# Performance work log

Hardware: AMD Instinct MI355X
Metric: run time of the kernel (lower is better)

The kernel has to match this reference:

```python
import jax, jax.numpy as jnp
import numpy as np

VOCAB = 50000
EMB = 200        # embedding_size
CAP = 3          # capitalization_size
IN = EMB + CAP   # LSTM input size = 203
HID = 128        # LSTMCell(128)
B = 256
T = 500          # comment_length
NC = 6           # num_classes
DENSE = 64


def _lstm_scan(x_tbi, W, b):
    """x_tbi: [T,B,IN]. W: [IN+HID, 4*HID] (tf gate order i, j, f, o), b: [4*HID].
    Returns h sequence [T,B,HID]. forget_bias=1.0 as in tf.contrib.rnn.LSTMCell."""
    h0 = jnp.zeros((x_tbi.shape[1], HID), x_tbi.dtype)

    def step(carry, x):
        h, c = carry
        gates = jnp.concatenate([x, h], axis=-1) @ W + b   # [B, 4*HID]
        i, j, f, o = jnp.split(gates, 4, axis=-1)
        c = jax.nn.sigmoid(f + 1.0) * c + jax.nn.sigmoid(i) * jnp.tanh(j)
        h = jax.nn.sigmoid(o) * jnp.tanh(c)
        return (h, c), h

    _, hs = jax.lax.scan(step, (h0, h0), x_tbi)
    return hs


def setup_inputs() -> dict:
    key = jax.random.key(0)
    ks = jax.random.split(key, 12)
    words = jax.random.randint(ks[0], (B, T), 0, VOCAB, dtype=jnp.int32)
    capitals = jax.random.randint(ks[1], (B, T), 0, CAP, dtype=jnp.int32)
    # word embeddings: random trainable table with a trailing zero-padding row
    word_emb = jax.random.normal(ks[2], (VOCAB + 1, EMB), dtype=jnp.float32) * 0.1
    # capitalization embedding: one_hot_embedding_matrix(3) = [eye(3); zeros(1,3)]
    cap_emb = jnp.concatenate([jnp.eye(CAP, dtype=jnp.float32),
                               jnp.zeros((1, CAP), dtype=jnp.float32)], axis=0)
    def glorot(k, shape):
        lim = np.sqrt(6.0 / (shape[0] + shape[1]))
        return jax.random.uniform(k, shape, jnp.float32, -lim, lim)
    W_fw = glorot(ks[3], (IN + HID, 4 * HID))
    b_fw = jnp.zeros((4 * HID,), jnp.float32)
    W_bw = glorot(ks[4], (IN + HID, 4 * HID))
    b_bw = jnp.zeros((4 * HID,), jnp.float32)
    W1 = glorot(ks[5], (2 * HID, DENSE))
    b1 = jnp.zeros((DENSE,), jnp.float32)
    W2 = glorot(ks[6], (DENSE, NC))
    b2 = jnp.zeros((NC,), jnp.float32)
    return {"words": words, "capitals": capitals, "word_emb": word_emb,
            "cap_emb": cap_emb, "W_fw": W_fw, "b_fw": b_fw,
            "W_bw": W_bw, "b_bw": b_bw, "W1": W1, "b1": b1,
            "W2": W2, "b2": b2}


def reference(words, capitals, word_emb, cap_emb, W_fw, b_fw, W_bw, b_bw,
              W1, b1, W2, b2):
    # embedding lookups and concat -> [B, T, 203]
    x = jnp.concatenate([word_emb[words], cap_emb[capitals]], axis=-1)
    x_tbi = jnp.transpose(x, (1, 0, 2))                    # [T, B, IN]
    # forward direction: take output at last timestep
    h_fw_last = _lstm_scan(x_tbi, W_fw, b_fw)[-1]          # [B, HID]
    # backward direction: bidirectional_dynamic_rnn reverses bw outputs back,
    # so outputs[1][:, 0, :] == last state of scan over the reversed sequence
    h_bw_first = _lstm_scan(x_tbi[::-1], W_bw, b_bw)[-1]   # [B, HID]
    rnn_output = jnp.concatenate([h_fw_last, h_bw_first], axis=1)  # [B, 256]
    dense1 = jax.nn.elu(rnn_output @ W1 + b1)              # [B, 64]
    y_hat = jax.nn.sigmoid(dense1 @ W2 + b2)               # [B, NC]
    return y_hat
```

## Files before the change

kernel.cpp:

```cpp
#include <hip/hip_runtime.h>

#define T 500
#define NB 256
#define VROWS 50001
#define EMB 200
#define KPAD 224
#define LOG2E 1.44269504f

typedef unsigned short u16;
typedef __attribute__((ext_vector_type(8))) __bf16 bf16x8;
typedef __attribute__((ext_vector_type(8))) short short8;
typedef __attribute__((ext_vector_type(8))) u16 u16x8;
typedef __attribute__((ext_vector_type(4))) float f32x4;
typedef __attribute__((ext_vector_type(4))) u16 u16x4;

__device__ __forceinline__ u16 f2bf(float x) {
  __bf16 h = (__bf16)x;
  return __builtin_bit_cast(u16, h);
}
__device__ __forceinline__ float bf2f(u16 b) {
  union { unsigned u; float f; } v; v.u = ((unsigned)b) << 16;
  return v.f;
}
__device__ __forceinline__ float rcp_(float x) { return __builtin_amdgcn_rcpf(x); }
__device__ __forceinline__ float ex2_(float x) { return __builtin_amdgcn_exp2f(x); }
__device__ __forceinline__ float gsc(int g) { return (g == 1) ? 2.f * LOG2E : -LOG2E; }

__global__ void prep_kernel(const float* __restrict__ cap_emb,
                            const float* __restrict__ Wfw, const float* __restrict__ bfw,
                            const float* __restrict__ Wbw, const float* __restrict__ bbw,
                            float* __restrict__ Cproj, u16* __restrict__ Bt) {
  const int S2 = 2 * 512 * KPAD;
  const int S3 = 2 * 4 * 512;
  int tid = blockIdx.x * blockDim.x + threadIdx.x;
  int nthr = gridDim.x * blockDim.x;
  for (int i = tid; i < S2 + S3; i += nthr) {
    if (i < S2) {
      int d = i / (512 * KPAD), rem = i - d * (512 * KPAD);
      int colp = rem / KPAD, k = rem - colp * KPAD;
      const float* W = d ? Wbw : Wfw;
      int g = colp & 3, jj = colp >> 2;
      Bt[i] = (k < EMB) ? f2bf(W[k * 512 + g * 128 + jj] * gsc(g)) : (u16)0;
    } else {
      int idx = i - S2;
      int dir = idx >> 11; int c = (idx >> 9) & 3; int colp = idx & 511;
      int j = colp >> 2, g = colp & 3;
      const float* W = dir ? Wbw : Wfw;
      const float* bias = dir ? bbw : bfw;
      float v = bias[g * 128 + j] + (g == 2 ? 1.f : 0.f);
      #pragma unroll
      for (int cc = 0; cc < 3; ++cc)
        v += cap_emb[c * 3 + cc] * W[(200 + cc) * 512 + g * 128 + j];
      Cproj[idx] = v * gsc(g);
    }
  }
}

__global__ __launch_bounds__(256) void xproj_kernel(
    const int* __restrict__ words, const int* __restrict__ caps,
    const float* __restrict__ word_emb, const u16* __restrict__ Bt,
    const float* __restrict__ Cproj, u16* __restrict__ XP) {
  const int mt = blockIdx.x, nt = blockIdx.y, dir = blockIdx.z;
  const u16* __restrict__ B = Bt + (size_t)dir * 512 * KPAD;
  const float* __restrict__ Cb = Cproj + dir * 4 * 512;
  u16* __restrict__ xp = XP + (size_t)dir * T * NB * 512;

  __shared__ u16 As[2][128 * 32];
  __shared__ u16 Bs[2][128 * 32];

  const int tid = threadIdx.x;
  const int w = tid >> 6, l = tid & 63;
  const int la = l & 15, lb = l >> 4;
  const int m0 = mt * 128, n0 = nt * 128;
  const int tblk = m0 >> 8;

  const int ar = tid >> 1, ah = tid & 1;
  const int ab = (m0 & 255) + ar;
  const int aword = words[ab * T + tblk];
  const float* __restrict__ aemb = word_emb + (size_t)aword * EMB;

  auto stageA = [&](int buf, int ks) {
    int kbase = ks * 32 + ah * 16;
    u16x8 lo, hi;
    #pragma unroll
    for (int q = 0; q < 4; ++q) {
      int k = kbase + q * 4;
      f32x4 v;
      if (k < EMB) v = *(const f32x4*)(aemb + k);
      else v = f32x4{0.f, 0.f, 0.f, 0.f};
      u16 b0 = f2bf(v[0]), b1 = f2bf(v[1]), b2 = f2bf(v[2]), b3 = f2bf(v[3]);
      if (q < 2) { lo[q*4+0]=b0; lo[q*4+1]=b1; lo[q*4+2]=b2; lo[q*4+3]=b3; }
      else { int qq=q-2; hi[qq*4+0]=b0; hi[qq*4+1]=b1; hi[qq*4+2]=b2; hi[qq*4+3]=b3; }
    }
    *(u16x8*)&As[buf][ar * 32 + ah * 16]     = lo;
    *(u16x8*)&As[buf][ar * 32 + ah * 16 + 8] = hi;
  };
  auto stageB = [&](int buf, int ks) {
    int k0 = ks * 32;
    #pragma unroll
    for (int h = 0; h < 2; ++h) {
      int c = w * 128 + h * 64 + l;
      int row = c >> 2, kq = c & 3;
      const u16* gb = B + (size_t)(n0 + row) * KPAD + k0 + kq * 8;
      __builtin_amdgcn_global_load_lds(
          (const __attribute__((address_space(1))) void*)gb,
          (__attribute__((address_space(3))) void*)&Bs[buf][(w * 128 + h * 64) * 8],
          16, 0, 0);
    }
  };

  f32x4 z = {0.f, 0.f, 0.f, 0.f};
  f32x4 acc[4][4] = {{z,z,z,z},{z,z,z,z},{z,z,z,z},{z,z,z,z}};
  const int wr = w >> 1, wc = w & 1;

  stageA(0, 0); stageB(0, 0);
  __syncthreads();
  #pragma unroll 1
  for (int ks = 0; ks < 7; ++ks) {
    int cur = ks & 1;
    if (ks < 6) { stageA(cur ^ 1, ks + 1); stageB(cur ^ 1, ks + 1); }
    bf16x8 af[4], bfr[4];
    #pragma unroll
    for (int m = 0; m < 4; ++m)
      af[m] = *(const bf16x8*)&As[cur][(wr * 64 + m * 16 + la) * 32 + lb * 8];
    #pragma unroll
    for (int n = 0; n < 4; ++n)
      bfr[n] = *(const bf16x8*)&Bs[cur][(wc * 64 + n * 16 + la) * 32 + lb * 8];
    #pragma unroll
    for (int m = 0; m < 4; ++m)
      #pragma unroll
      for (int n = 0; n < 4; ++n)
        acc[m][n] = __builtin_amdgcn_mfma_f32_16x16x32_bf16(af[m], bfr[n], acc[m][n], 0, 0, 0);
    __syncthreads();
  }

  #pragma unroll
  for (int m = 0; m < 4; ++m) {
    #pragma unroll
    for (int r = 0; r < 4; ++r) {
      int b = (m0 & 255) + wr * 64 + m * 16 + lb * 4 + r;
      int cap = caps[b * T + tblk];
      const float* cbr = Cb + cap * 512;
      u16* op = xp + ((size_t)tblk * NB + b) * 512;
      #pragma unroll
      for (int n = 0; n < 4; ++n) {
        int colp = n0 + wc * 64 + n * 16 + la;
        op[colp] = f2bf(acc[m][n][r] + cbr[colp]);
      }
    }
  }
}

template <int PAR>
__device__ __forceinline__ void lstm_step(
    int t, int dir, int la, int lb, int j,
    const u16* __restrict__ xpd, int voff0, int voff1, int voff2, int voff3,
    const bf16x8 (&bfrag)[4][4], u16* __restrict__ hbuf,
    u16x4 (&xc)[4],
    u16x4 (&xg)[4],
    f32x4& cst, f32x4& hl) {
  const u16* hb = hbuf + PAR * 2048;
  const int swz = (la & 7) << 3;
  bf16x8 afr[4];
  #pragma unroll
  for (int kk = 0; kk < 4; ++kk)
    afr[kk] = *(const bf16x8*)(hb + ((la * 128 + kk * 32 + lb * 8) ^ swz));

  {
    int ts = t + 2; if (ts > T - 1) ts = T - 1;
    int tt = dir ? (T - 1 - ts) : ts;
    const u16* p = xpd + (size_t)tt * (NB * 512);
    xg[0] = *(const u16x4*)(p + voff0);
    xg[1] = *(const u16x4*)(p + voff1);
    xg[2] = *(const u16x4*)(p + voff2);
    xg[3] = *(const u16x4*)(p + voff3);
  }

  f32x4 acc0, acc1, acc2, acc3;
  #pragma unroll
  for (int r = 0; r < 4; ++r) {
    acc0[r] = bf2f(xc[r][0]);
    acc1[r] = bf2f(xc[r][1]);
    acc2[r] = bf2f(xc[r][2]);
    acc3[r] = bf2f(xc[r][3]);
  }
  __builtin_amdgcn_s_setprio(1);
  #pragma unroll
  for (int kk = 0; kk < 4; ++kk) {
    acc0 = __builtin_amdgcn_mfma_f32_16x16x32_bf16(afr[kk], bfrag[0][kk], acc0, 0, 0, 0);
    acc1 = __builtin_amdgcn_mfma_f32_16x16x32_bf16(afr[kk], bfrag[1][kk], acc1, 0, 0, 0);
    acc2 = __builtin_amdgcn_mfma_f32_16x16x32_bf16(afr[kk], bfrag[2][kk], acc2, 0, 0, 0);
    acc3 = __builtin_amdgcn_mfma_f32_16x16x32_bf16(afr[kk], bfrag[3][kk], acc3, 0, 0, 0);
  }
  __builtin_amdgcn_s_setprio(0);
  u16* ho = hbuf + (PAR ^ 1) * 2048;
  #pragma unroll
  for (int r = 0; r < 4; ++r) {
    float ig = rcp_(1.f + ex2_(acc0[r]));
    float tj = 1.f - 2.f * rcp_(1.f + ex2_(acc1[r]));
    float fg = rcp_(1.f + ex2_(acc2[r]));
    float cn = fg * cst[r] + ig * tj;
    cst[r] = cn;
    float og = rcp_(1.f + ex2_(acc3[r]));
    float hn = og * (1.f - 2.f * rcp_(1.f + ex2_(2.f * LOG2E * cn)));
    hl[r] = hn;
    int row = lb * 4 + r;
    ho[(row * 128 + j) ^ ((row & 7) << 3)] = f2bf(hn);
  }
  __builtin_amdgcn_sched_barrier(0);
  asm volatile("s_waitcnt lgkmcnt(0)");
  __builtin_amdgcn_s_barrier();
  __builtin_amdgcn_sched_barrier(0);
}

__global__ __launch_bounds__(512, 1) void lstm_kernel(
    const u16* __restrict__ XP, const float* __restrict__ Wfw,
    const float* __restrict__ Wbw, float* __restrict__ rnn) {
  const int dir = blockIdx.x & 1;
  const int chunk = blockIdx.x >> 1;
  const int b0 = chunk * 16;
  const u16* __restrict__ xpd = XP + (size_t)dir * T * NB * 512;
  const float* __restrict__ W = dir ? Wbw : Wfw;

  const int tid = threadIdx.x;
  const int w = tid >> 6, l = tid & 63, la = l & 15, lb = l >> 4;
  const int j = w * 16 + la;

  const int voff0 = (b0 + lb * 4 + 0) * 512 + j * 4;
  const int voff1 = (b0 + lb * 4 + 1) * 512 + j * 4;
  const int voff2 = (b0 + lb * 4 + 2) * 512 + j * 4;
  const int voff3 = (b0 + lb * 4 + 3) * 512 + j * 4;

  bf16x8 bfrag[4][4];
  #pragma unroll
  for (int g = 0; g < 4; ++g) {
    #pragma unroll
    for (int kk = 0; kk < 4; ++kk) {
      short8 t8;
      #pragma unroll
      for (int r = 0; r < 8; ++r) {
        int k = kk * 32 + lb * 8 + r;
        t8[r] = (short)f2bf(W[(203 + k) * 512 + g * 128 + j] * gsc(g));
      }
      bfrag[g][kk] = __builtin_bit_cast(bf16x8, t8);
    }
  }

  __shared__ u16 hbuf[2 * 16 * 128];
  for (int i = tid; i < 2 * 16 * 128; i += 512) hbuf[i] = 0;

  f32x4 cst = {0.f, 0.f, 0.f, 0.f};
  f32x4 hl  = {0.f, 0.f, 0.f, 0.f};

  u16x4 xA[4], xB[4], xC[4], xD[4];
  {
    int tt0 = dir ? (T - 1) : 0;
    int tt1 = dir ? (T - 2) : 1;
    const u16* p0 = xpd + (size_t)tt0 * (NB * 512);
    const u16* p1 = xpd + (size_t)tt1 * (NB * 512);
    xA[0] = *(const u16x4*)(p0 + voff0); xA[1] = *(const u16x4*)(p0 + voff1);
    xA[2] = *(const u16x4*)(p0 + voff2); xA[3] = *(const u16x4*)(p0 + voff3);
    xB[0] = *(const u16x4*)(p1 + voff0); xB[1] = *(const u16x4*)(p1 + voff1);
    xB[2] = *(const u16x4*)(p1 + voff2); xB[3] = *(const u16x4*)(p1 + voff3);
  }
  __syncthreads();

  #pragma unroll 1
  for (int tq = 0; tq < T / 4; ++tq) {
    int t0 = 4 * tq;
    lstm_step<0>(t0,     dir, la, lb, j, xpd, voff0, voff1, voff2, voff3,
                 bfrag, hbuf, xA, xC, cst, hl);
    lstm_step<1>(t0 + 1, dir, la, lb, j, xpd, voff0, voff1, voff2, voff3,
                 bfrag, hbuf, xB, xD, cst, hl);
    lstm_step<0>(t0 + 2, dir, la, lb, j, xpd, voff0, voff1, voff2, voff3,
                 bfrag, hbuf, xC, xA, cst, hl);
    lstm_step<1>(t0 + 3, dir, la, lb, j, xpd, voff0, voff1, voff2, voff3,
                 bfrag, hbuf, xD, xB, cst, hl);
  }

  #pragma unroll
  for (int r = 0; r < 4; ++r)
    rnn[(size_t)(b0 + lb * 4 + r) * 256 + dir * 128 + j] = hl[r];
}

__global__ void head_kernel(const float* __restrict__ rnn, const float* __restrict__ W1,
                            const float* __restrict__ b1, const float* __restrict__ W2,
                            const float* __restrict__ b2, float* __restrict__ out) {
  int b = blockIdx.x;
  int jj = threadIdx.x;
  __shared__ float d1[64];
  float acc = b1[jj];
  const float* r = rnn + b * 256;
  #pragma unroll 4
  for (int k = 0; k < 256; ++k) acc += r[k] * W1[k * 64 + jj];
  d1[jj] = acc > 0.f ? acc : (__expf(acc) - 1.f);
  __syncthreads();
  if (jj < 6) {
    float a2 = b2[jj];
    #pragma unroll 8
    for (int k = 0; k < 64; ++k) a2 += d1[k] * W2[k * 6 + jj];
    out[b * 6 + jj] = rcp_(1.f + __expf(-a2));
  }
}

extern "C" void kernel_launch(void* const* d_in, const int* in_sizes, int n_in,
                              void* d_out, int out_size, void* d_ws, size_t ws_size,
                              hipStream_t stream) {
  (void)in_sizes; (void)n_in; (void)out_size; (void)ws_size;
  const int*   words    = (const int*)  d_in[0];
  const int*   caps     = (const int*)  d_in[1];
  const float* word_emb = (const float*)d_in[2];
  const float* cap_emb  = (const float*)d_in[3];
  const float* Wfw      = (const float*)d_in[4];
  const float* bfw      = (const float*)d_in[5];
  const float* Wbw      = (const float*)d_in[6];
  const float* bbw      = (const float*)d_in[7];
  const float* W1       = (const float*)d_in[8];
  const float* b1       = (const float*)d_in[9];
  const float* W2       = (const float*)d_in[10];
  const float* b2       = (const float*)d_in[11];
  float* out = (float*)d_out;

  char* base = (char*)d_ws;
  size_t off = 0;
  auto alloc = [&](size_t bytes) {
    char* q = base + off;
    off = (off + bytes + 255) & ~(size_t)255;
    return q;
  };
  u16*   XP     = (u16*)  alloc((size_t)2 * T * NB * 512 * 2);
  u16*   Bt     = (u16*)  alloc((size_t)2 * 512 * KPAD * 2);
  float* Cproj  = (float*)alloc((size_t)2 * 4 * 512 * 4);
  float* rnn    = (float*)alloc((size_t)256 * 256 * 4);

  hipLaunchKernelGGL(prep_kernel, dim3(256), dim3(256), 0, stream,
                     cap_emb, Wfw, bfw, Wbw, bbw, Cproj, Bt);
  hipLaunchKernelGGL(xproj_kernel, dim3(1000, 4, 2), dim3(256), 0, stream,
                     words, caps, word_emb, Bt, Cproj, XP);
  hipLaunchKernelGGL(lstm_kernel, dim3(32), dim3(512), 0, stream,
                     XP, Wfw, Wbw, rnn);
  hipLaunchKernelGGL(head_kernel, dim3(256), dim3(64), 0, stream,
                     rnn, W1, b1, W2, b2, out);
}
```

Before: 700.7 us.

## Pre-convert embeddings to bf16, stage A via async LDS loads, coalesce XP stores

The prep kernel now converts the whole word embedding table to a padded bf16 copy in workspace. The projection GEMM can then gather A rows with global_load_lds instead of per-thread fp32 loads and conversions, and it stages the accumulators through shared memory so each thread writes contiguous 16-byte chunks of XP. The LSTM cell math is also restructured to use fewer reciprocals per step, by combining the sigmoid and tanh denominators. This costs a full-table conversion on every call plus extra shared memory and barriers in the epilogue, and it falls back to the old kernel when the workspace is too small.

```diff
diff --git a/kernel.cpp b/kernel.cpp
--- a/kernel.cpp
+++ b/kernel.cpp
@@ -5,6 +5,7 @@
 #define VROWS 50001
 #define EMB 200
 #define KPAD 224
+#define MPAD 50048
 #define LOG2E 1.44269504f
 
 typedef unsigned short u16;
@@ -14,6 +15,9 @@
 typedef __attribute__((ext_vector_type(4))) float f32x4;
 typedef __attribute__((ext_vector_type(4))) u16 u16x4;
 
+#define AS1 __attribute__((address_space(1)))
+#define AS3 __attribute__((address_space(3)))
+
 __device__ __forceinline__ u16 f2bf(float x) {
   __bf16 h = (__bf16)x;
   return __builtin_bit_cast(u16, h);
@@ -27,9 +31,11 @@
 __device__ __forceinline__ float gsc(int g) { return (g == 1) ? 2.f * LOG2E : -LOG2E; }
 
 __global__ void prep_kernel(const float* __restrict__ cap_emb,
+                            const float* __restrict__ word_emb,
                             const float* __restrict__ Wfw, const float* __restrict__ bfw,
                             const float* __restrict__ Wbw, const float* __restrict__ bbw,
-                            float* __restrict__ Cproj, u16* __restrict__ Bt) {
+                            float* __restrict__ Cproj, u16* __restrict__ Bt,
+                            u16* __restrict__ Apad) {
   const int S2 = 2 * 512 * KPAD;
   const int S3 = 2 * 4 * 512;
   int tid = blockIdx.x * blockDim.x + threadIdx.x;
@@ -54,9 +60,126 @@
       Cproj[idx] = v * gsc(g);
     }
   }
+  if (Apad) {
+    const int S1 = MPAD * (KPAD / 4);
+    for (int i = tid; i < S1; i += nthr) {
+      int v = i / (KPAD / 4), q = i - v * (KPAD / 4);
+      int k = q * 4;
+      u16x4 o;
+      if (v < VROWS && k < EMB) {
+        const float* p = word_emb + (size_t)v * EMB + k;
+        o[0] = f2bf(p[0]); o[1] = f2bf(p[1]); o[2] = f2bf(p[2]); o[3] = f2bf(p[3]);
+      } else {
+        o[0] = o[1] = o[2] = o[3] = 0;
+      }
+      *(u16x4*)(Apad + (size_t)v * KPAD + k) = o;
+    }
+  }
 }
 
 __global__ __launch_bounds__(256) void xproj_kernel(
+    const int* __restrict__ words, const int* __restrict__ caps,
+    const u16* __restrict__ Apad, const u16* __restrict__ Bt,
+    const float* __restrict__ Cproj, u16* __restrict__ XP) {
+  const int mt = blockIdx.x, nt = blockIdx.y, dir = blockIdx.z;
+  const u16* __restrict__ B = Bt + (size_t)dir * 512 * KPAD;
+  u16* __restrict__ xp = XP + (size_t)dir * T * NB * 512;
+
+  __shared__ u16 As[2][128 * 32];
+  __shared__ u16 Bs[2][128 * 32];
+  __shared__ float Cls[64][132];
+
+  const int tid = threadIdx.x;
+  const int w = tid >> 6, l = tid & 63;
+  const int la = l & 15, lb = l >> 4;
+  const int m0 = mt * 128, n0 = nt * 128;
+  const int tblk = m0 >> 8;
+  const int bbase = m0 & 255;
+
+  const int c0 = w * 128 + l, c1 = w * 128 + 64 + l;
+  const int row0 = c0 >> 2, kq0 = c0 & 3;
+  const int row1 = c1 >> 2, kq1 = c1 & 3;
+  const int wd0 = words[(bbase + row0) * T + tblk];
+  const int wd1 = words[(bbase + row1) * T + tblk];
+  const u16* srcA0 = Apad + (size_t)wd0 * KPAD + kq0 * 8;
+  const u16* srcA1 = Apad + (size_t)wd1 * KPAD + kq1 * 8;
+
+  auto stage = [&](int buf, int ks) {
+    __builtin_amdgcn_global_load_lds(
+        (const AS1 void*)(srcA0 + ks * 32),
+        (AS3 void*)&As[buf][(w * 128) * 8], 16, 0, 0);
+    __builtin_amdgcn_global_load_lds(
+        (const AS1 void*)(srcA1 + ks * 32),
+        (AS3 void*)&As[buf][(w * 128 + 64) * 8], 16, 0, 0);
+    int k0 = ks * 32;
+    #pragma unroll
+    for (int h = 0; h < 2; ++h) {
+      int c = w * 128 + h * 64 + l;
+      int row = c >> 2, kq = c & 3;
+      const u16* gb = B + (size_t)(n0 + row) * KPAD + k0 + kq * 8;
+      __builtin_amdgcn_global_load_lds(
+          (const AS1 void*)gb,
+          (AS3 void*)&Bs[buf][(w * 128 + h * 64) * 8], 16, 0, 0);
+    }
+  };
+
+  f32x4 z = {0.f, 0.f, 0.f, 0.f};
+  f32x4 acc[4][4] = {{z,z,z,z},{z,z,z,z},{z,z,z,z},{z,z,z,z}};
+  const int wr = w >> 1, wc = w & 1;
+
+  stage(0, 0);
+  __syncthreads();
+  #pragma unroll 1
+  for (int ks = 0; ks < 7; ++ks) {
+    int cur = ks & 1;
+    if (ks < 6) stage(cur ^ 1, ks + 1);
+    bf16x8 af[4], bfr[4];
+    #pragma unroll
+    for (int m = 0; m < 4; ++m)
+      af[m] = *(const bf16x8*)&As[cur][(wr * 64 + m * 16 + la) * 32 + lb * 8];
+    #pragma unroll
+    for (int n = 0; n < 4; ++n)
+      bfr[n] = *(const bf16x8*)&Bs[cur][(wc * 64 + n * 16 + la) * 32 + lb * 8];
+    #pragma unroll
+    for (int m = 0; m < 4; ++m)
+      #pragma unroll
+      for (int n = 0; n < 4; ++n)
+        acc[m][n] = __builtin_amdgcn_mfma_f32_16x16x32_bf16(af[m], bfr[n], acc[m][n], 0, 0, 0);
+    __syncthreads();
+  }
+
+  const int rrow = tid >> 1, rch = tid & 1;
+  const int rb = bbase + rrow;
+  const int rcap = caps[rb * T + tblk];
+  const float* __restrict__ cbase = Cproj + (dir * 4 + rcap) * 512;
+  u16* __restrict__ rop = xp + ((size_t)tblk * NB + rb) * 512;
+
+  #pragma unroll
+  for (int pass = 0; pass < 2; ++pass) {
+    if (wc == pass) {
+      #pragma unroll
+      for (int m = 0; m < 4; ++m)
+        #pragma unroll
+        for (int n = 0; n < 4; ++n)
+          *(f32x4*)&Cls[n * 16 + la][wr * 64 + m * 16 + lb * 4] = acc[m][n];
+    }
+    __syncthreads();
+    int colp0 = n0 + pass * 64 + rch * 32;
+    #pragma unroll
+    for (int s = 0; s < 4; ++s) {
+      u16x8 o;
+      #pragma unroll
+      for (int e = 0; e < 8; ++e) {
+        int cl = rch * 32 + s * 8 + e;
+        o[e] = f2bf(Cls[cl][rrow] + cbase[colp0 + s * 8 + e]);
+      }
+      *(u16x8*)(rop + colp0 + s * 8) = o;
+    }
+    __syncthreads();
+  }
+}
+
+__global__ __launch_bounds__(256) void xproj_fb_kernel(
     const int* __restrict__ words, const int* __restrict__ caps,
     const float* __restrict__ word_emb, const u16* __restrict__ Bt,
     const float* __restrict__ Cproj, u16* __restrict__ XP) {
@@ -64,21 +187,17 @@
   const u16* __restrict__ B = Bt + (size_t)dir * 512 * KPAD;
   const float* __restrict__ Cb = Cproj + dir * 4 * 512;
   u16* __restrict__ xp = XP + (size_t)dir * T * NB * 512;
-
   __shared__ u16 As[2][128 * 32];
   __shared__ u16 Bs[2][128 * 32];
-
   const int tid = threadIdx.x;
   const int w = tid >> 6, l = tid & 63;
   const int la = l & 15, lb = l >> 4;
   const int m0 = mt * 128, n0 = nt * 128;
   const int tblk = m0 >> 8;
-
   const int ar = tid >> 1, ah = tid & 1;
   const int ab = (m0 & 255) + ar;
   const int aword = words[ab * T + tblk];
   const float* __restrict__ aemb = word_emb + (size_t)aword * EMB;
-
   auto stageA = [&](int buf, int ks) {
     int kbase = ks * 32 + ah * 16;
     u16x8 lo, hi;
@@ -103,16 +222,13 @@
       int row = c >> 2, kq = c & 3;
       const u16* gb = B + (size_t)(n0 + row) * KPAD + k0 + kq * 8;
       __builtin_amdgcn_global_load_lds(
-          (const __attribute__((address_space(1))) void*)gb,
-          (__attribute__((address_space(3))) void*)&Bs[buf][(w * 128 + h * 64) * 8],
-          16, 0, 0);
+          (const AS1 void*)gb,
+          (AS3 void*)&Bs[buf][(w * 128 + h * 64) * 8], 16, 0, 0);
     }
   };
-
   f32x4 z = {0.f, 0.f, 0.f, 0.f};
   f32x4 acc[4][4] = {{z,z,z,z},{z,z,z,z},{z,z,z,z},{z,z,z,z}};
   const int wr = w >> 1, wc = w & 1;
-
   stageA(0, 0); stageB(0, 0);
   __syncthreads();
   #pragma unroll 1
@@ -133,7 +249,6 @@
         acc[m][n] = __builtin_amdgcn_mfma_f32_16x16x32_bf16(af[m], bfr[n], acc[m][n], 0, 0, 0);
     __syncthreads();
   }
-
   #pragma unroll
   for (int m = 0; m < 4; ++m) {
     #pragma unroll
@@ -196,13 +311,15 @@
   u16* ho = hbuf + (PAR ^ 1) * 2048;
   #pragma unroll
   for (int r = 0; r < 4; ++r) {
-    float ig = rcp_(1.f + ex2_(acc0[r]));
-    float tj = 1.f - 2.f * rcp_(1.f + ex2_(acc1[r]));
-    float fg = rcp_(1.f + ex2_(acc2[r]));
-    float cn = fg * cst[r] + ig * tj;
+    float ei = ex2_(acc0[r]);
+    float ej = ex2_(acc1[r]);
+    float ef = ex2_(acc2[r]);
+    float eo = ex2_(acc3[r]);
+    float itj = (ej - 1.f) * rcp_((1.f + ei) * (1.f + ej));
+    float cn = cst[r] * rcp_(1.f + ef) + itj;
     cst[r] = cn;
-    float og = rcp_(1.f + ex2_(acc3[r]));
-    float hn = og * (1.f - 2.f * rcp_(1.f + ex2_(2.f * LOG2E * cn)));
+    float E = ex2_(2.f * LOG2E * cn);
+    float hn = (E - 1.f) * rcp_((1.f + eo) * (1.f + E));
     hl[r] = hn;
     int row = lb * 4 + r;
     ho[(row * 128 + j) ^ ((row & 7) << 3)] = f2bf(hn);
@@ -306,7 +423,7 @@
 extern "C" void kernel_launch(void* const* d_in, const int* in_sizes, int n_in,
                               void* d_out, int out_size, void* d_ws, size_t ws_size,
                               hipStream_t stream) {
-  (void)in_sizes; (void)n_in; (void)out_size; (void)ws_size;
+  (void)in_sizes; (void)n_in; (void)out_size;
   const int*   words    = (const int*)  d_in[0];
   const int*   caps     = (const int*)  d_in[1];
   const float* word_emb = (const float*)d_in[2];
@@ -332,11 +449,20 @@
   u16*   Bt     = (u16*)  alloc((size_t)2 * 512 * KPAD * 2);
   float* Cproj  = (float*)alloc((size_t)2 * 4 * 512 * 4);
   float* rnn    = (float*)alloc((size_t)256 * 256 * 4);
-
-  hipLaunchKernelGGL(prep_kernel, dim3(256), dim3(256), 0, stream,
-                     cap_emb, Wfw, bfw, Wbw, bbw, Cproj, Bt);
-  hipLaunchKernelGGL(xproj_kernel, dim3(1000, 4, 2), dim3(256), 0, stream,
-                     words, caps, word_emb, Bt, Cproj, XP);
+  size_t off_no_apad = off;
+  u16*   Apad   = (u16*)  alloc((size_t)MPAD * KPAD * 2);
+  bool use_apad = (off <= ws_size);
+  if (!use_apad) { Apad = nullptr; off = off_no_apad; }
+
+  hipLaunchKernelGGL(prep_kernel, dim3(2048), dim3(256), 0, stream,
+                     cap_emb, word_emb, Wfw, bfw, Wbw, bbw, Cproj, Bt, Apad);
+  if (use_apad) {
+    hipLaunchKernelGGL(xproj_kernel, dim3(1000, 4, 2), dim3(256), 0, stream,
+                       words, caps, Apad, Bt, Cproj, XP);
+  } else {
+    hipLaunchKernelGGL(xproj_fb_kernel, dim3(1000, 4, 2), dim3(256), 0, stream,
+                       words, caps, word_emb, Bt, Cproj, XP);
+  }
   hipLaunchKernelGGL(lstm_kernel, dim3(32), dim3(512), 0, stream,
                      XP, Wfw, Wbw, rnn);
   hipLaunchKernelGGL(head_kernel, dim3(256), dim3(64), 0, stream,
```

Result: no change. 696.1 us (-0.7%).
